# Optimization experiments

Hardware: AMD Instinct MI355X
Metric: run time of the kernel (lower is better)

Reference implementation:

```python
import jax, jax.numpy as jnp
import numpy as np

B, C, F, T = 4, 64, 128, 128
K = 8        # kernel_size
H = 32       # lstm hidden size
L = 4        # lstm layers
EPS = 1e-5


def setup_inputs() -> dict:
    key = jax.random.key(0)
    ks = jax.random.split(key, 12)
    f = lambda k, s: jax.random.normal(k, s, dtype=jnp.float32) * 0.1
    return dict(
        x=jax.random.normal(ks[0], (B, C, F, T), dtype=jnp.float32),
        gamma=jnp.ones((C,), jnp.float32),
        beta=jnp.zeros((C,), jnp.float32),
        # layer 0 (input size C*K), stacked over 2 directions
        w_ih0=f(ks[1], (2, 4 * H, C * K)),
        w_hh0=f(ks[2], (2, 4 * H, H)),
        b_ih0=f(ks[3], (2, 4 * H)),
        b_hh0=f(ks[4], (2, 4 * H)),
        # layers 1..L-1 (input size 2*H), stacked [L-1, 2dirs, ...]
        w_ih=f(ks[5], (L - 1, 2, 4 * H, 2 * H)),
        w_hh=f(ks[6], (L - 1, 2, 4 * H, H)),
        b_ih=f(ks[7], (L - 1, 2, 4 * H)),
        b_hh=f(ks[8], (L - 1, 2, 4 * H)),
        # ConvTranspose1d weight, torch layout [in=2H, out=C, K]
        wct=f(ks[9], (2 * H, C, K)),
        bct=f(ks[10], (C,)),
    )


def _lstm_dir(gx, whh, reverse):
    # gx: [S, N, 4H] precomputed input projections (+ both biases)
    Hh = whh.shape[1]
    N = gx.shape[1]

    def step(carry, g):
        h, c = carry
        g = g + h @ whh.T
        i, fg, gg, o = jnp.split(g, 4, axis=-1)  # torch gate order i,f,g,o
        c = jax.nn.sigmoid(fg) * c + jax.nn.sigmoid(i) * jnp.tanh(gg)
        h = jax.nn.sigmoid(o) * jnp.tanh(c)
        return (h, c), h

    init = (jnp.zeros((N, Hh), gx.dtype), jnp.zeros((N, Hh), gx.dtype))
    _, hs = jax.lax.scan(step, init, gx, reverse=reverse)
    return hs  # [S, N, H], time-aligned with input


def _bilstm(xs, wih, whh, bih, bhh):
    outs = []
    for d, rev in ((0, False), (1, True)):
        gx = jnp.einsum('sni,gi->sng', xs, wih[d]) + bih[d] + bhh[d]
        outs.append(_lstm_dir(gx, whh[d], rev))
    return jnp.concatenate(outs, axis=-1)  # [S, N, 2H]


def reference(x, gamma, beta, w_ih0, w_hh0, b_ih0, b_hh0,
              w_ih, w_hh, b_ih, b_hh, wct, bct):
    x = jnp.swapaxes(x, -1, -2)  # [B, C, T, F]
    res = x
    Bb, Cc, Tt, Ff = x.shape
    # InstanceNorm2d (affine, biased variance over (T,F))
    mu = jnp.mean(x, axis=(2, 3), keepdims=True)
    var = jnp.var(x, axis=(2, 3), keepdims=True)
    xn = (x - mu) * jax.lax.rsqrt(var + EPS)
    xn = xn * gamma[None, :, None, None] + beta[None, :, None, None]
    # [B,F,C,T] -> [B*F, C, T]
    xf = jnp.transpose(xn, (0, 3, 1, 2)).reshape(Bb * Ff, Cc, Tt)
    # unfold(dim=2, size=K, step=1): [BF, C, T', K]
    Tp = Tt - K + 1
    idx = jnp.arange(Tp)[:, None] + jnp.arange(K)[None, :]
    seq = jnp.transpose(xf[:, :, idx], (2, 0, 1, 3)).reshape(Tp, Bb * Ff, Cc * K)
    # 4-layer bidirectional LSTM
    h = _bilstm(seq, w_ih0, w_hh0, b_ih0, b_hh0)
    for l in range(w_ih.shape[0]):
        h = _bilstm(h, w_ih[l], w_hh[l], b_ih[l], b_hh[l])
    # [S, BF, 2H] -> [BF, 2H, S]
    h = jnp.transpose(h, (1, 2, 0))
    # ConvTranspose1d stride=1, pad=0: out length = S + K - 1 = T
    y = jax.lax.conv_transpose(
        h, wct, strides=(1,), padding='VALID',
        dimension_numbers=('NCH', 'IOH', 'NCH'), transpose_kernel=True)
    y = y + bct[None, :, None]
    y = y.reshape(Bb, Ff, Cc, Tt)
    y = jnp.transpose(y, (0, 2, 3, 1)) + res  # [B, C, T, F]
    return jnp.swapaxes(y, -1, -2)  # back to [B, C, F, T]
```

## Files before the change

kernel.cpp:

```cpp
#include <hip/hip_runtime.h>

#define B_ 4
#define C_ 64
#define F_ 128
#define T_ 128
#define K_ 8
#define H_ 32
#define S_ 121
#define N_ 512
#define G_ 128
#define CK_ 512

typedef __attribute__((ext_vector_type(8))) short short8;
typedef __attribute__((ext_vector_type(4))) float f32x4;
typedef __attribute__((ext_vector_type(2))) float f32x2;
typedef __attribute__((ext_vector_type(2))) unsigned int ui2;
union FragU { uint4 u; short8 s; };

__device__ __forceinline__ unsigned int pk2(float a, float b){
  unsigned int ua = __float_as_uint(a); ua += 0x7fffu + ((ua>>16)&1u);
  unsigned int ub = __float_as_uint(b); ub += 0x7fffu + ((ub>>16)&1u);
  return (ua>>16) | (ub & 0xffff0000u);
}
__device__ __forceinline__ unsigned short bfu(float a){
  unsigned int ua = __float_as_uint(a); ua += 0x7fffu + ((ua>>16)&1u);
  return (unsigned short)(ua>>16);
}

__device__ __forceinline__ int gslot(int g){ return ((g & 63) << 1) | (g >> 6); }

__global__ __launch_bounds__(256) void k_prep(const float* __restrict__ x,
    const float* __restrict__ gamma, const float* __restrict__ beta,
    float* __restrict__ scale, float* __restrict__ shift,
    const float* __restrict__ wih0, unsigned short* __restrict__ wb0,
    const float* __restrict__ wih, unsigned short* __restrict__ wlb,
    const float* __restrict__ wct, unsigned short* __restrict__ wcv){
  int blk = blockIdx.x;
  if (blk < 512){
    int i = blk*256 + threadIdx.x;
    wb0[i] = bfu(wih0[i]);
  } else if (blk < 704){
    int i = (blk - 512)*256 + threadIdx.x;
    wlb[i] = bfu(wih[i]);
  } else if (blk < 832){
    int i = (blk - 704)*256 + threadIdx.x;
    int jx = (i & ~7) | (7 - (i & 7));
    wcv[i] = bfu(wct[jx]);
  } else {
    int bc = blk - 832;
    const float* p = x + (size_t)bc * (F_*T_);
    float s = 0.f, q = 0.f;
    for (int i = threadIdx.x; i < F_*T_; i += 256){ float v = p[i]; s += v; q += v*v; }
    #pragma unroll
    for (int o = 32; o; o >>= 1){ s += __shfl_down(s, o); q += __shfl_down(q, o); }
    __shared__ float ss[4], qq[4];
    int w = threadIdx.x >> 6;
    if ((threadIdx.x & 63) == 0){ ss[w] = s; qq[w] = q; }
    __syncthreads();
    if (threadIdx.x == 0){
      s = ss[0]+ss[1]+ss[2]+ss[3]; q = qq[0]+qq[1]+qq[2]+qq[3];
      float mu  = s / (float)(F_*T_);
      float var = q / (float)(F_*T_) - mu*mu;
      if (var < 0.f) var = 0.f;
      int c = bc & (C_-1);
      float sc = gamma[c] * rsqrtf(var + 1e-5f);
      scale[bc] = sc;
      shift[bc] = beta[c] - mu * sc;
    }
  }
}

__global__ __launch_bounds__(256) void k_gx0(const float* __restrict__ x,
    const float* __restrict__ scale, const float* __restrict__ shift,
    const unsigned short* __restrict__ wb0, const float* __restrict__ bi,
    const float* __restrict__ bh, unsigned short* __restrict__ gx){
  __shared__ unsigned int xsp[C_][80];
  __shared__ unsigned int glb[64][68];
  int n = blockIdx.x >> 1, half = blockIdx.x & 1;
  int b = n >> 7, f = n & 127;
  const float* xb = x + (size_t)b*C_*F_*T_ + (size_t)f*T_;
  for (int i = threadIdx.x; i < C_*18; i += 256){
    int c = i / 18, q = i - c*18;
    int t0 = half*64 + q*4;
    float sc = scale[b*C_+c], sh = shift[b*C_+c];
    const float* xr = xb + (size_t)c*F_*T_;
    float4 v = (float4){0.f,0.f,0.f,0.f};
    float e = 0.f;
    bool in4 = (t0 < T_);
    if (in4) v = *(const float4*)(xr + t0);
    if (t0 + 4 < T_) e = xr[t0 + 4];
    float u0 = in4 ? v.x*sc+sh : 0.f;
    float u1 = in4 ? v.y*sc+sh : 0.f;
    float u2 = in4 ? v.z*sc+sh : 0.f;
    float u3 = in4 ? v.w*sc+sh : 0.f;
    float u4 = (t0+4 < T_) ? e*sc+sh : 0.f;
    unsigned int* xc = &xsp[c][q*4];
    xc[0] = pk2(u0,u1); xc[1] = pk2(u1,u2); xc[2] = pk2(u2,u3); xc[3] = pk2(u3,u4);
  }
  __syncthreads();
  int lane = threadIdx.x & 63, wv = threadIdx.x >> 6;
  int ln = lane & 15, quad = lane >> 4;
  int g256[4]; f32x4 acc[4][4];
  #pragma unroll
  for (int gi = 0; gi < 4; ++gi){
    g256[gi] = (wv*4 + gi)*16 + ln;
    float bv = bi[g256[gi]] + bh[g256[gi]];
    #pragma unroll
    for (int stl = 0; stl < 4; ++stl) acc[stl][gi] = (f32x4){bv, bv, bv, bv};
  }
  FragU bq0[4], bq1[4], bq2[4];
  #pragma unroll
  for (int gi = 0; gi < 4; ++gi){
    bq0[gi].u = *(const uint4*)(wb0 + (size_t)g256[gi]*CK_ + quad*8);
    bq1[gi].u = *(const uint4*)(wb0 + (size_t)g256[gi]*CK_ + 32 + quad*8);
  }
  #pragma unroll
  for (int kb = 0; kb < 16; ++kb){
    FragU* bu = (kb % 3 == 0) ? bq0 : (kb % 3 == 1) ? bq1 : bq2;
    FragU* bl = ((kb+2) % 3 == 0) ? bq0 : ((kb+2) % 3 == 1) ? bq1 : bq2;
    if (kb < 14){
      #pragma unroll
      for (int gi = 0; gi < 4; ++gi)
        bl[gi].u = *(const uint4*)(wb0 + (size_t)g256[gi]*CK_ + (kb+2)*32 + quad*8);
    }
    #pragma unroll
    for (int stl = 0; stl < 4; ++stl){
      FragU a;
      const unsigned int* rp = &xsp[kb*4 + quad][stl*16 + ln];
      a.u.x = rp[0]; a.u.y = rp[2]; a.u.z = rp[4]; a.u.w = rp[6];
      #pragma unroll
      for (int gi = 0; gi < 4; ++gi)
        acc[stl][gi] = __builtin_amdgcn_mfma_f32_16x16x32_bf16(a.s, bu[gi].s, acc[stl][gi], 0, 0, 0);
    }
  }
  unsigned short* gl16 = (unsigned short*)&glb[0][0];
  for (int pass = 0; pass < 2; ++pass){
    if ((wv >> 1) == pass){
      #pragma unroll
      for (int stl = 0; stl < 4; ++stl)
        #pragma unroll
        for (int gi = 0; gi < 4; ++gi){
          int slot = gslot(g256[gi] & 127);
          #pragma unroll
          for (int r = 0; r < 4; ++r){
            int srow = stl*16 + quad*4 + r;
            gl16[srow*136 + slot] = bfu(acc[stl][gi][r]);
          }
        }
    }
    __syncthreads();
    for (int q = threadIdx.x; q < 1024; q += 256){
      int srow = q >> 4, col = q & 15;
      int s = half*64 + srow;
      if (s < S_){
        uint4 v = *(const uint4*)(&glb[srow][col*4]);
        *(uint4*)(gx + ((size_t)(pass*N_ + n)*S_ + s)*G_ + col*8) = v;
      }
    }
    __syncthreads();
  }
}

__global__ __launch_bounds__(128)
__attribute__((amdgpu_waves_per_eu(1, 1)))
void k_mega(const unsigned short* __restrict__ gx,
    const float* __restrict__ whh0,
    const unsigned short* __restrict__ wlb,
    const float* __restrict__ bih, const float* __restrict__ bhh,
    const float* __restrict__ whh,
    const unsigned short* __restrict__ wcv,
    const float* __restrict__ bct,
    const float* __restrict__ x,
    float* __restrict__ out){
  __shared__ unsigned int smem[17280];
  unsigned int (*rawA)[68]     = (unsigned int (*)[68])smem;
  unsigned int (*rawB)[68]     = (unsigned int (*)[68])(smem + 4352);
  unsigned int (*glds)[32][66] = (unsigned int (*)[32][66])(smem + 8704);
  unsigned int (*hsp)[136]     = (unsigned int (*)[136])(smem + 12928);
  unsigned int (*hp2h)[136]    = (unsigned int (*)[136])smem;

  int n = blockIdx.x, b = n >> 7, f = n & 127;
  int tid = threadIdx.x;
  int lane = tid & 63, d = tid >> 6;
  int j = lane & 31, hi = lane >> 5;
  int ln = lane & 15, quad = lane >> 4;

  f32x2 w1[16], w2[16];
  float hv = 0.f, c = 0.f;
  unsigned int hgd[4];
  auto step = [&](unsigned int cur, int u){
    float gg1 = __uint_as_float(cur << 16);
    float gg2 = __uint_as_float(cur & 0xffff0000u);
    f32x2 A1 = {gg1, 0.f}, B1 = {0.f, 0.f};
    f32x2 A2 = {gg2, 0.f}, B2 = {0.f, 0.f};
    #pragma unroll
    for (int m = 0; m < 16; m += 2){
      f32x2 h0, h1;
      h0.x = __uint_as_float(__builtin_amdgcn_readlane(__float_as_uint(hv), 2*m));
      h0.y = __uint_as_float(__builtin_amdgcn_readlane(__float_as_uint(hv), 2*m+1));
      h1.x = __uint_as_float(__builtin_amdgcn_readlane(__float_as_uint(hv), 2*m+2));
      h1.y = __uint_as_float(__builtin_amdgcn_readlane(__float_as_uint(hv), 2*m+3));
      A1 += h0*w1[m];   A2 += h0*w2[m];
      B1 += h1*w1[m+1]; B2 += h1*w2[m+1];
    }
    float acc1 = (A1.x + B1.x) + (A1.y + B1.y);
    float acc2 = (A2.x + B2.x) + (A2.y + B2.y);
    float a1 = 1.f/(1.f + __expf(-acc1));
    float x2 = hi ? acc2 : 2.f*acc2;
    float tt = 1.f/(1.f + __expf(-x2));
    float a2 = hi ? tt : 2.f*tt - 1.f;
    ui2 p1 = __builtin_amdgcn_permlane32_swap(__float_as_uint(a1), __float_as_uint(a1), false, false);
    ui2 p2 = __builtin_amdgcn_permlane32_swap(__float_as_uint(a2), __float_as_uint(a2), false, false);
    float i_ = __uint_as_float(p1.x);
    float f_ = __uint_as_float(p1.y);
    float g_ = __uint_as_float(p2.x);
    float o_ = __uint_as_float(p2.y);
    c = f_*c + i_*g_;
    float tc = 1.f/(1.f + __expf(-2.f*c));
    hv = o_*(2.f*tc - 1.f);
    unsigned int hb = (unsigned int)bfu(hv);
    if ((u & 1) == 0) hgd[u >> 1] = hb;
    else              hgd[u >> 1] |= hb << 16;
  };
  auto loadw = [&](const float* wr1, const float* wr2){
    #pragma unroll
    for (int q = 0; q < 8; ++q){
      float4 aa = *(const float4*)(wr1 + q*4);
      float4 bb = *(const float4*)(wr2 + q*4);
      w1[q*2+0] = (f32x2){aa.x, aa.y}; w1[q*2+1] = (f32x2){aa.z, aa.w};
      w2[q*2+0] = (f32x2){bb.x, bb.y}; w2[q*2+1] = (f32x2){bb.z, bb.w};
    }
    #pragma unroll
    for (int k = 0; k < 16; ++k){
      asm volatile("" : "+v"(w1[k]));
      asm volatile("" : "+v"(w2[k]));
    }
  };

  {
    loadw(whh0 + (size_t)(d*G_ + lane)*H_, whh0 + (size_t)(d*G_ + lane + 64)*H_);
    const unsigned int* gxu = (const unsigned int*)gx;
    ptrdiff_t stride = d ? -64 : 64;
    const unsigned int* p0 = gxu + ((size_t)(d*N_ + n)*S_ + (d ? (S_-1) : 0))*64 + lane;
    unsigned short* hrow = (unsigned short*)&rawA[d*32 + j][0];
    unsigned int bufA[8], bufB[8];
    #pragma unroll
    for (int u = 0; u < 8; ++u) bufA[u] = p0[stride*u];
    for (int gg = 0; gg < 7; ++gg){
      int g0 = gg*2;
      #pragma unroll
      for (int u = 0; u < 8; ++u) bufB[u] = p0[stride*(8*(g0+1) + u)];
      #pragma unroll
      for (int u = 0; u < 8; ++u) step(bufA[u], u);
      if (!hi) *(uint4*)(hrow + 8*g0) = (uint4){hgd[0], hgd[1], hgd[2], hgd[3]};
      #pragma unroll
      for (int u = 0; u < 8; ++u) bufA[u] = p0[stride*(8*(g0+2) + u)];
      #pragma unroll
      for (int u = 0; u < 8; ++u) step(bufB[u], u);
      if (!hi) *(uint4*)(hrow + 8*(g0+1)) = (uint4){hgd[0], hgd[1], hgd[2], hgd[3]};
    }
    bufB[0] = p0[stride*120];
    #pragma unroll
    for (int u = 0; u < 8; ++u) step(bufA[u], u);
    if (!hi) *(uint4*)(hrow + 112) = (uint4){hgd[0], hgd[1], hgd[2], hgd[3]};
    step(bufB[0], 0);
    if (!hi) hrow[120] = (unsigned short)(hgd[0] & 0xffffu);
  }
  __syncthreads();

  unsigned int (*rin)[68]  = rawA;
  unsigned int (*rout)[68] = rawB;
  for (int l = 0; l < 3; ++l){
    const unsigned short* rawu = (const unsigned short*)&rin[0][0];
    for (int i = tid; i < 32*128; i += 128){
      int srow = i >> 5, ip = i & 31;
      unsigned int v = 0;
      if (srow <= 120){
        int st = (ip < 16) ? srow : (120 - srow);
        v = (unsigned int)rawu[(2*ip)*136 + st] | ((unsigned int)rawu[(2*ip+1)*136 + st] << 16);
      }
      hsp[ip][srow] = v;
    }
    __syncthreads();

    const unsigned short* wp = wlb + (size_t)((l*2 + d)*G_)*64;
    float bias[8];
    const float* bip = bih + (size_t)(l*2 + d)*G_;
    const float* bhp = bhh + (size_t)(l*2 + d)*G_;
    #pragma unroll
    for (int gt = 0; gt < 8; ++gt) bias[gt] = bip[gt*16 + ln] + bhp[gt*16 + ln];
    loadw(whh + (size_t)((l*2 + d)*G_ + lane)*H_,
          whh + (size_t)((l*2 + d)*G_ + lane + 64)*H_);

    FragU bfrc[8][2];
    #pragma unroll
    for (int gt = 0; gt < 8; ++gt){
      bfrc[gt][0].u = *(const uint4*)(wp + (size_t)(gt*16 + ln)*64 + quad*8);
      bfrc[gt][1].u = *(const uint4*)(wp + (size_t)(gt*16 + ln)*64 + 32 + quad*8);
    }

    unsigned short* hrow = (unsigned short*)&rout[d*32 + j][0];
    const unsigned int* gr = &glds[d][0][lane];
    hv = 0.f; c = 0.f;

    for (int ch = 0; ch < 4; ++ch){
      int c0 = d ? (89 - 32*ch) : (32*ch);
      FragU af[2][2];
      #pragma unroll
      for (int stl = 0; stl < 2; ++stl){
        int srow = c0 + stl*16 + ln; if (srow < 0) srow = 0;
        #pragma unroll
        for (int kb = 0; kb < 2; ++kb){
          int ipb = kb*16 + quad*4;
          af[stl][kb].u.x = hsp[ipb+0][srow];
          af[stl][kb].u.y = hsp[ipb+1][srow];
          af[stl][kb].u.z = hsp[ipb+2][srow];
          af[stl][kb].u.w = hsp[ipb+3][srow];
        }
      }
      #pragma unroll
      for (int stl = 0; stl < 2; ++stl)
        #pragma unroll
        for (int gt2 = 0; gt2 < 4; ++gt2){
          f32x4 alo = (f32x4){bias[gt2],   bias[gt2],   bias[gt2],   bias[gt2]};
          f32x4 ahi = (f32x4){bias[gt2+4], bias[gt2+4], bias[gt2+4], bias[gt2+4]};
          alo = __builtin_amdgcn_mfma_f32_16x16x32_bf16(af[stl][0].s, bfrc[gt2  ][0].s, alo, 0, 0, 0);
          alo = __builtin_amdgcn_mfma_f32_16x16x32_bf16(af[stl][1].s, bfrc[gt2  ][1].s, alo, 0, 0, 0);
          ahi = __builtin_amdgcn_mfma_f32_16x16x32_bf16(af[stl][0].s, bfrc[gt2+4][0].s, ahi, 0, 0, 0);
          ahi = __builtin_amdgcn_mfma_f32_16x16x32_bf16(af[stl][1].s, bfrc[gt2+4][1].s, ahi, 0, 0, 0);
          #pragma unroll
          for (int r = 0; r < 4; ++r){
            int off = stl*16 + quad*4 + r;
            int ul = d ? (31 - off) : off;
            glds[d][ul][gt2*16 + ln] = pk2(alo[r], ahi[r]);
          }
        }
      asm volatile("" ::: "memory");
      int nfull = (ch < 3) ? 4 : 3;
      for (int gq = 0; gq < nfull; ++gq){
        unsigned int bv[8];
        #pragma unroll
        for (int u = 0; u < 8; ++u) bv[u] = gr[(gq*8 + u)*66];
        #pragma unroll
        for (int u = 0; u < 8; ++u) step(bv[u], u);
        if (!hi) *(uint4*)(hrow + ch*32 + gq*8) = (uint4){hgd[0], hgd[1], hgd[2], hgd[3]};
      }
      if (ch == 3){
        unsigned int bv0 = gr[24*66];
        step(bv0, 0);
        if (!hi) hrow[120] = (unsigned short)(hgd[0] & 0xffffu);
      }
      asm volatile("" ::: "memory");
    }
    __syncthreads();
    unsigned int (*t)[68] = rin; rin = rout; rout = t;
  }

  {
    f32x4 ac[2][8];
    #pragma unroll
    for (int cg = 0; cg < 2; ++cg)
      #pragma unroll
      for (int nt = 0; nt < 8; ++nt) ac[cg][nt] = (f32x4){0.f,0.f,0.f,0.f};
    const unsigned short* wp0 = wcv + (size_t)(d*32 + ln)*512;
    const unsigned short* wp1 = wcv + (size_t)(d*32 + 16 + ln)*512;
    const unsigned short* rawu2 = (const unsigned short*)&rin[0][0];
    for (int pass = 0; pass < 2; ++pass){
      for (int it = tid; it < 32*136; it += 128){
        int cil = it / 136, col = it - cil*136;
        int ci = pass*32 + cil;
        int t0 = col - 8;
        int i0 = (ci < 32) ? t0 : (120 - t0);
        int i1 = (ci < 32) ? (t0+1) : (119 - t0);
        unsigned int lo  = (t0   >= 0 && t0   <= 120) ? rawu2[ci*136 + i0] : 0u;
        unsigned int hi2 = (t0+1 >= 0 && t0+1 <= 120) ? rawu2[ci*136 + i1] : 0u;
        hp2h[cil][col] = lo | (hi2 << 16);
      }
      __syncthreads();
      for (int kb = pass*8; kb < pass*8 + 8; ++kb){
        FragU a0, a1;
        a0.u = *(const uint4*)(wp0 + kb*32 + quad*8);
        a1.u = *(const uint4*)(wp1 + kb*32 + quad*8);
        int cil = (kb - pass*8)*4 + quad;
        #pragma unroll
        for (int nt = 0; nt < 8; ++nt){
          FragU bfr;
          const unsigned int* rp = &hp2h[cil][nt*16 + ln + 1];
          bfr.u.x = rp[0]; bfr.u.y = rp[2]; bfr.u.z = rp[4]; bfr.u.w = rp[6];
          ac[0][nt] = __builtin_amdgcn_mfma_f32_16x16x32_bf16(a0.s, bfr.s, ac[0][nt], 0, 0, 0);
          ac[1][nt] = __builtin_amdgcn_mfma_f32_16x16x32_bf16(a1.s, bfr.s, ac[1][nt], 0, 0, 0);
        }
      }
      __syncthreads();
    }
    #pragma unroll
    for (int cg = 0; cg < 2; ++cg){
      float bb[4];
      #pragma unroll
      for (int r = 0; r < 4; ++r) bb[r] = bct[d*32 + cg*16 + quad*4 + r];
      #pragma unroll
      for (int nt = 0; nt < 8; ++nt)
        #pragma unroll
        for (int r = 0; r < 4; ++r){
          int co = d*32 + cg*16 + quad*4 + r, t = nt*16 + ln;
          size_t idx = ((size_t)(b*64 + co)*128 + f)*128 + t;
          out[idx] = ac[cg][nt][r] + bb[r] + x[idx];
        }
    }
  }
}

extern "C" void kernel_launch(void* const* d_in, const int* in_sizes, int n_in,
                              void* d_out, int out_size, void* d_ws, size_t ws_size,
                              hipStream_t stream){
  const float* x     = (const float*)d_in[0];
  const float* gamma = (const float*)d_in[1];
  const float* beta  = (const float*)d_in[2];
  const float* wih0  = (const float*)d_in[3];
  const float* whh0  = (const float*)d_in[4];
  const float* bih0  = (const float*)d_in[5];
  const float* bhh0  = (const float*)d_in[6];
  const float* wih   = (const float*)d_in[7];
  const float* whh   = (const float*)d_in[8];
  const float* bih   = (const float*)d_in[9];
  const float* bhh   = (const float*)d_in[10];
  const float* wct   = (const float*)d_in[11];
  const float* bct   = (const float*)d_in[12];
  float* out = (float*)d_out;

  char* wsb = (char*)d_ws;
  float*          scale = (float*)(wsb);
  float*          shift = (float*)(wsb + 1024);
  unsigned short* gx    = (unsigned short*)(wsb + 2048);
  unsigned short* wb0   = (unsigned short*)(wsb + 48498688);
  unsigned short* wlb   = (unsigned short*)(wsb + 48760832);
  unsigned short* wcv   = (unsigned short*)(wsb + 48859136);

  k_prep<<<1088, 256, 0, stream>>>(x, gamma, beta, scale, shift,
                                   wih0, wb0, wih, wlb, wct, wcv);
  k_gx0 <<<1024, 256, 0, stream>>>(x, scale, shift, wb0, bih0, bhh0, gx);
  k_mega<<<512, 128, 0, stream>>>(gx, whh0, wlb, bih, bhh, whh, wcv, bct, x, out);
}
```

Before: 326.4 us.

## Compute LSTM recurrent matvec with bf16 MFMA instead of readlane FMA loop

The per-step recurrent h·W_hh product in the fused LSTM kernel now runs as bf16 MFMA 16x16x32 instructions instead of a scalar loop of readlane broadcasts and packed FMAs. The hidden state is written to a small LDS buffer each step and read back as an MFMA operand, and W_hh is pre-converted to bf16 in the prep kernel. This is meant to shorten the serial latency chain of each timestep. In exchange it adds an LDS round trip per step, discards most MFMA outputs through lane selection, and lowers the recurrent weights to bf16, which loses some precision.

```diff
diff --git a/kernel.cpp b/kernel.cpp
--- a/kernel.cpp
+++ b/kernel.cpp
@@ -13,7 +13,6 @@
 
 typedef __attribute__((ext_vector_type(8))) short short8;
 typedef __attribute__((ext_vector_type(4))) float f32x4;
-typedef __attribute__((ext_vector_type(2))) float f32x2;
 typedef __attribute__((ext_vector_type(2))) unsigned int ui2;
 union FragU { uint4 u; short8 s; };
 
@@ -34,7 +33,9 @@
     float* __restrict__ scale, float* __restrict__ shift,
     const float* __restrict__ wih0, unsigned short* __restrict__ wb0,
     const float* __restrict__ wih, unsigned short* __restrict__ wlb,
-    const float* __restrict__ wct, unsigned short* __restrict__ wcv){
+    const float* __restrict__ wct, unsigned short* __restrict__ wcv,
+    const float* __restrict__ whh0, unsigned short* __restrict__ whh0b,
+    const float* __restrict__ whh, unsigned short* __restrict__ whhlb){
   int blk = blockIdx.x;
   if (blk < 512){
     int i = blk*256 + threadIdx.x;
@@ -46,8 +47,14 @@
     int i = (blk - 704)*256 + threadIdx.x;
     int jx = (i & ~7) | (7 - (i & 7));
     wcv[i] = bfu(wct[jx]);
+  } else if (blk < 864){
+    int i = (blk - 832)*256 + threadIdx.x;
+    whh0b[i] = bfu(whh0[i]);
+  } else if (blk < 960){
+    int i = (blk - 864)*256 + threadIdx.x;
+    whhlb[i] = bfu(whh[i]);
   } else {
-    int bc = blk - 832;
+    int bc = blk - 960;
     const float* p = x + (size_t)bc * (F_*T_);
     float s = 0.f, q = 0.f;
     for (int i = threadIdx.x; i < F_*T_; i += 256){ float v = p[i]; s += v; q += v*v; }
@@ -164,15 +171,15 @@
 __global__ __launch_bounds__(128)
 __attribute__((amdgpu_waves_per_eu(1, 1)))
 void k_mega(const unsigned short* __restrict__ gx,
-    const float* __restrict__ whh0,
+    const unsigned short* __restrict__ whh0b,
     const unsigned short* __restrict__ wlb,
     const float* __restrict__ bih, const float* __restrict__ bhh,
-    const float* __restrict__ whh,
+    const unsigned short* __restrict__ whhlb,
     const unsigned short* __restrict__ wcv,
     const float* __restrict__ bct,
     const float* __restrict__ x,
     float* __restrict__ out){
-  __shared__ unsigned int smem[17280];
+  __shared__ unsigned int smem[17312];
   unsigned int (*rawA)[68]     = (unsigned int (*)[68])smem;
   unsigned int (*rawB)[68]     = (unsigned int (*)[68])(smem + 4352);
   unsigned int (*glds)[32][66] = (unsigned int (*)[32][66])(smem + 8704);
@@ -185,26 +192,41 @@
   int j = lane & 31, hi = lane >> 5;
   int ln = lane & 15, quad = lane >> 4;
 
-  f32x2 w1[16], w2[16];
+  unsigned short* hbp16 = (unsigned short*)(smem + 17280 + d*16);
+  const uint4*    hbq   = (const uint4*)(smem + 17280 + d*16) + quad;
+
+  FragU wb[8];
   float hv = 0.f, c = 0.f;
   unsigned int hgd[4];
+  auto loadwb = [&](const unsigned short* whhb){
+    #pragma unroll
+    for (int t = 0; t < 8; ++t)
+      wb[t].u = *(const uint4*)(whhb + (size_t)(t*16 + ln)*H_ + quad*8);
+    #pragma unroll
+    for (int t = 0; t < 8; ++t)
+      asm volatile("" : "+v"(wb[t].u.x), "+v"(wb[t].u.y), "+v"(wb[t].u.z), "+v"(wb[t].u.w));
+  };
+  auto hzero = [&](){
+    hv = 0.f; c = 0.f;
+    if (!hi) hbp16[j] = 0;
+    asm volatile("" ::: "memory");
+  };
   auto step = [&](unsigned int cur, int u){
-    float gg1 = __uint_as_float(cur << 16);
-    float gg2 = __uint_as_float(cur & 0xffff0000u);
-    f32x2 A1 = {gg1, 0.f}, B1 = {0.f, 0.f};
-    f32x2 A2 = {gg2, 0.f}, B2 = {0.f, 0.f};
-    #pragma unroll
-    for (int m = 0; m < 16; m += 2){
-      f32x2 h0, h1;
-      h0.x = __uint_as_float(__builtin_amdgcn_readlane(__float_as_uint(hv), 2*m));
-      h0.y = __uint_as_float(__builtin_amdgcn_readlane(__float_as_uint(hv), 2*m+1));
-      h1.x = __uint_as_float(__builtin_amdgcn_readlane(__float_as_uint(hv), 2*m+2));
-      h1.y = __uint_as_float(__builtin_amdgcn_readlane(__float_as_uint(hv), 2*m+3));
-      A1 += h0*w1[m];   A2 += h0*w2[m];
-      B1 += h1*w1[m+1]; B2 += h1*w2[m+1];
-    }
-    float acc1 = (A1.x + B1.x) + (A1.y + B1.y);
-    float acc2 = (A2.x + B2.x) + (A2.y + B2.y);
+    asm volatile("" ::: "memory");
+    FragU af; af.u = *hbq;
+    f32x4 z4 = (f32x4){0.f,0.f,0.f,0.f};
+    f32x4 m0 = __builtin_amdgcn_mfma_f32_16x16x32_bf16(af.s, wb[0].s, z4, 0,0,0);
+    f32x4 m1 = __builtin_amdgcn_mfma_f32_16x16x32_bf16(af.s, wb[1].s, z4, 0,0,0);
+    f32x4 m2 = __builtin_amdgcn_mfma_f32_16x16x32_bf16(af.s, wb[2].s, z4, 0,0,0);
+    f32x4 m3 = __builtin_amdgcn_mfma_f32_16x16x32_bf16(af.s, wb[3].s, z4, 0,0,0);
+    f32x4 m4 = __builtin_amdgcn_mfma_f32_16x16x32_bf16(af.s, wb[4].s, z4, 0,0,0);
+    f32x4 m5 = __builtin_amdgcn_mfma_f32_16x16x32_bf16(af.s, wb[5].s, z4, 0,0,0);
+    f32x4 m6 = __builtin_amdgcn_mfma_f32_16x16x32_bf16(af.s, wb[6].s, z4, 0,0,0);
+    f32x4 m7 = __builtin_amdgcn_mfma_f32_16x16x32_bf16(af.s, wb[7].s, z4, 0,0,0);
+    float r1 = (quad==0) ? m0[0] : (quad==1) ? m1[0] : (quad==2) ? m2[0] : m3[0];
+    float r2 = (quad==0) ? m4[0] : (quad==1) ? m5[0] : (quad==2) ? m6[0] : m7[0];
+    float acc1 = __uint_as_float(cur << 16)          + r1;
+    float acc2 = __uint_as_float(cur & 0xffff0000u)  + r2;
     float a1 = 1.f/(1.f + __expf(-acc1));
     float x2 = hi ? acc2 : 2.f*acc2;
     float tt = 1.f/(1.f + __expf(-x2));
@@ -219,26 +241,15 @@
     float tc = 1.f/(1.f + __expf(-2.f*c));
     hv = o_*(2.f*tc - 1.f);
     unsigned int hb = (unsigned int)bfu(hv);
+    if (!hi) hbp16[j] = (unsigned short)hb;
+    asm volatile("" ::: "memory");
     if ((u & 1) == 0) hgd[u >> 1] = hb;
     else              hgd[u >> 1] |= hb << 16;
   };
-  auto loadw = [&](const float* wr1, const float* wr2){
-    #pragma unroll
-    for (int q = 0; q < 8; ++q){
-      float4 aa = *(const float4*)(wr1 + q*4);
-      float4 bb = *(const float4*)(wr2 + q*4);
-      w1[q*2+0] = (f32x2){aa.x, aa.y}; w1[q*2+1] = (f32x2){aa.z, aa.w};
-      w2[q*2+0] = (f32x2){bb.x, bb.y}; w2[q*2+1] = (f32x2){bb.z, bb.w};
-    }
-    #pragma unroll
-    for (int k = 0; k < 16; ++k){
-      asm volatile("" : "+v"(w1[k]));
-      asm volatile("" : "+v"(w2[k]));
-    }
-  };
 
   {
-    loadw(whh0 + (size_t)(d*G_ + lane)*H_, whh0 + (size_t)(d*G_ + lane + 64)*H_);
+    loadwb(whh0b + (size_t)d*G_*H_);
+    hzero();
     const unsigned int* gxu = (const unsigned int*)gx;
     ptrdiff_t stride = d ? -64 : 64;
     const unsigned int* p0 = gxu + ((size_t)(d*N_ + n)*S_ + (d ? (S_-1) : 0))*64 + lane;
@@ -289,8 +300,7 @@
     const float* bhp = bhh + (size_t)(l*2 + d)*G_;
     #pragma unroll
     for (int gt = 0; gt < 8; ++gt) bias[gt] = bip[gt*16 + ln] + bhp[gt*16 + ln];
-    loadw(whh + (size_t)((l*2 + d)*G_ + lane)*H_,
-          whh + (size_t)((l*2 + d)*G_ + lane + 64)*H_);
+    loadwb(whhlb + (size_t)(l*2 + d)*G_*H_);
 
     FragU bfrc[8][2];
     #pragma unroll
@@ -301,7 +311,7 @@
 
     unsigned short* hrow = (unsigned short*)&rout[d*32 + j][0];
     const unsigned int* gr = &glds[d][0][lane];
-    hv = 0.f; c = 0.f;
+    hzero();
 
     for (int ch = 0; ch < 4; ++ch){
       int c0 = d ? (89 - 32*ch) : (32*ch);
@@ -432,12 +442,15 @@
   float*          scale = (float*)(wsb);
   float*          shift = (float*)(wsb + 1024);
   unsigned short* gx    = (unsigned short*)(wsb + 2048);
+  unsigned short* whh0b = (unsigned short*)(wsb + 31721472);
+  unsigned short* whhlb = (unsigned short*)(wsb + 31737856);
   unsigned short* wb0   = (unsigned short*)(wsb + 48498688);
   unsigned short* wlb   = (unsigned short*)(wsb + 48760832);
   unsigned short* wcv   = (unsigned short*)(wsb + 48859136);
 
-  k_prep<<<1088, 256, 0, stream>>>(x, gamma, beta, scale, shift,
-                                   wih0, wb0, wih, wlb, wct, wcv);
+  k_prep<<<1216, 256, 0, stream>>>(x, gamma, beta, scale, shift,
+                                   wih0, wb0, wih, wlb, wct, wcv,
+                                   whh0, whh0b, whh, whhlb);
   k_gx0 <<<1024, 256, 0, stream>>>(x, scale, shift, wb0, bih0, bhh0, gx);
-  k_mega<<<512, 128, 0, stream>>>(gx, whh0, wlb, bih, bhh, whh, wcv, bct, x, out);
-}
+  k_mega<<<512, 128, 0, stream>>>(gx, whh0b, wlb, bih, bhh, whhlb, wcv, bct, x, out);
+}
```

Measured after the change: 343.8 us. 1.05x slower.
